# Performance work log

Measured on AMD Instinct MI355X. Metric: run time of the kernel, lower is better.

The kernel has to match this reference:

```python
import jax, jax.numpy as jnp
import numpy as np

B, T, D = 2, 2048, 2048
N_HEADS, N_KV = 16, 4
HD = D // N_HEADS  # 128
ROPE_BASE = 10000.0


def _rope_tables(t, dim, base=ROPE_BASE):
    inv_freq = 1.0 / (base ** (jnp.arange(0, dim, 2, dtype=jnp.float32) / dim))
    freqs = jnp.arange(t, dtype=jnp.float32)[:, None] * inv_freq[None, :]  # (T, dim/2)
    emb = jnp.concatenate([freqs, freqs], axis=-1)  # (T, dim)
    return jnp.cos(emb), jnp.sin(emb)


def _rotate_half(x):
    x1, x2 = jnp.split(x, 2, axis=-1)
    return jnp.concatenate([-x2, x1], axis=-1)


def _apply_rope(x, cos, sin):
    # x: (B, H, T, hd); cos/sin: (T, hd)
    return x * cos[None, None] + _rotate_half(x) * sin[None, None]


def setup_inputs() -> dict:
    key = jax.random.key(0)
    ks = jax.random.split(key, 5)
    s = 0.02
    return {
        "x": jax.random.normal(ks[0], (B, T, D), jnp.float32),
        "wq": jax.random.normal(ks[1], (D, N_HEADS * HD), jnp.float32) * s,
        "wk": jax.random.normal(ks[2], (D, N_KV * HD), jnp.float32) * s,
        "wv": jax.random.normal(ks[3], (D, N_KV * HD), jnp.float32) * s,
        "wo": jax.random.normal(ks[4], (D, D), jnp.float32) * s,
    }


def reference(x, wq, wk, wv, wo):
    b, t, c = x.shape
    n_rep = N_HEADS // N_KV
    scale = 1.0 / np.sqrt(HD)

    q = (x @ wq).reshape(b, t, N_HEADS, HD).transpose(0, 2, 1, 3)  # (B,H,T,hd)
    k = (x @ wk).reshape(b, t, N_KV, HD).transpose(0, 2, 1, 3)     # (B,Hkv,T,hd)
    v = (x @ wv).reshape(b, t, N_KV, HD).transpose(0, 2, 1, 3)

    cos, sin = _rope_tables(t, HD)
    q = _apply_rope(q, cos, sin)
    k = _apply_rope(k, cos, sin)

    # repeat_kv (GQA)
    k = jnp.repeat(k, n_rep, axis=1)  # (B,H,T,hd)
    v = jnp.repeat(v, n_rep, axis=1)

    scores = jnp.einsum("bhqd,bhkd->bhqk", q, k) * scale
    causal = jnp.tril(jnp.ones((t, t), dtype=bool))
    scores = jnp.where(causal[None, None], scores, -jnp.inf)
    attn = jax.nn.softmax(scores, axis=-1)
    out = jnp.einsum("bhqk,bhkd->bhqd", attn, v)
    out = out.transpose(0, 2, 1, 3).reshape(b, t, c)
    return out @ wo
```

## Files before the change

kernel.cpp:

```cpp
#include <hip/hip_runtime.h>
#include <hip/hip_bf16.h>
#include <math.h>

#define B_   2
#define T_   2048
#define D_   2048
#define NH_  16
#define NKV_ 4
#define HD_  128
#define MROWS (B_*T_)
#define NQKV  (NH_*HD_ + 2*NKV_*HD_)

typedef __bf16 bf16_t;
typedef __bf16 bf16x8 __attribute__((ext_vector_type(8)));
typedef __bf16 bf16x4 __attribute__((ext_vector_type(4)));
typedef float  floatx4 __attribute__((ext_vector_type(4)));

__device__ __forceinline__ void async_copy16(const bf16_t* gsrc, bf16_t* ldst) {
  __builtin_amdgcn_global_load_lds(
      (const __attribute__((address_space(1))) unsigned int*)gsrc,
      (__attribute__((address_space(3))) unsigned int*)ldst, 16, 0, 0);
}

__global__ void prep_fused(const float* __restrict__ s0, const float* __restrict__ s1,
                           const float* __restrict__ s2, const float* __restrict__ s3,
                           const float* __restrict__ sx,
                           bf16_t* __restrict__ d0, bf16_t* __restrict__ d1,
                           bf16_t* __restrict__ d2, bf16_t* __restrict__ d3,
                           bf16_t* __restrict__ dx) {
  const int z = blockIdx.z;
  const int tx = threadIdx.x, ty = threadIdx.y;
  if (z == 4) {
    int i = ((blockIdx.y * 64 + blockIdx.x) * 256 + ty * 32 + tx) * 8;
    float4 a = *(const float4*)(sx + i);
    float4 b = *(const float4*)(sx + i + 4);
    bf16x8 v;
    v[0]=(bf16_t)a.x; v[1]=(bf16_t)a.y; v[2]=(bf16_t)a.z; v[3]=(bf16_t)a.w;
    v[4]=(bf16_t)b.x; v[5]=(bf16_t)b.y; v[6]=(bf16_t)b.z; v[7]=(bf16_t)b.w;
    *(bf16x8*)(dx + i) = v;
    return;
  }
  const int N = (z == 1 || z == 2) ? 512 : 2048;
  const int n0 = blockIdx.x * 32;
  if (n0 >= N) return;
  const float* src = (z == 0) ? s0 : (z == 1) ? s1 : (z == 2) ? s2 : s3;
  bf16_t*      dst = (z == 0) ? d0 : (z == 1) ? d1 : (z == 2) ? d2 : d3;
  const int K = 2048;
  __shared__ float tile[32][33];
  int k0 = blockIdx.y * 32;
#pragma unroll
  for (int r = 0; r < 4; r++)
    tile[ty + r*8][tx] = src[(size_t)(k0 + ty + r*8) * N + n0 + tx];
  __syncthreads();
#pragma unroll
  for (int r = 0; r < 4; r++)
    dst[(size_t)(n0 + ty + r*8) * K + k0 + tx] = (bf16_t)tile[tx][ty + r*8];
}

template <typename OUT_T>
__global__ __launch_bounds__(256, 3)
void gemm_bt(const bf16_t* __restrict__ A, const bf16_t* __restrict__ Bt,
             OUT_T* __restrict__ C, int M, int N, int K) {
  __shared__ __align__(16) bf16_t As[128 * 64];
  __shared__ __align__(16) bf16_t Bs[128 * 64];
  const int tid  = threadIdx.x;
  const int wave = tid >> 6, lane = tid & 63;
  const int quad = lane >> 4, l16 = lane & 15;
  const int nBlocksM = M >> 7;
  const int bm = blockIdx.x % nBlocksM, bn = blockIdx.x / nBlocksM;
  const int m0 = bm * 128, n0 = bn * 128;
  const int wm = (wave >> 1) * 64, wn = (wave & 1) * 64;

  floatx4 acc[4][4];
#pragma unroll
  for (int i = 0; i < 4; i++)
#pragma unroll
    for (int j = 0; j < 4; j++) acc[i][j] = floatx4{0.f, 0.f, 0.f, 0.f};

  for (int k0 = 0; k0 < K; k0 += 64) {
    __syncthreads();
#pragma unroll
    for (int i = 0; i < 4; i++) {
      int e = i * 256 + tid;
      int row = e >> 3, grp = e & 7;
      int gg = grp ^ (row & 7);
      async_copy16(A + (size_t)(m0 + row) * K + k0 + gg * 8, As + e * 8);
    }
#pragma unroll
    for (int i = 0; i < 4; i++) {
      int e = i * 256 + tid;
      int row = e >> 3, grp = e & 7;
      int gg = grp ^ (row & 7);
      async_copy16(Bt + (size_t)(n0 + row) * K + k0 + gg * 8, Bs + e * 8);
    }
    __syncthreads();
#pragma unroll
    for (int ks = 0; ks < 2; ks++) {
      bf16x8 af[4], bfr[4];
      int grp = ks * 4 + quad;
#pragma unroll
      for (int mi = 0; mi < 4; mi++) {
        int row = wm + mi * 16 + l16;
        af[mi] = *(const bf16x8*)(As + row * 64 + ((grp ^ (row & 7)) << 3));
      }
#pragma unroll
      for (int ni = 0; ni < 4; ni++) {
        int row = wn + ni * 16 + l16;
        bfr[ni] = *(const bf16x8*)(Bs + row * 64 + ((grp ^ (row & 7)) << 3));
      }
#pragma unroll
      for (int mi = 0; mi < 4; mi++)
#pragma unroll
        for (int ni = 0; ni < 4; ni++)
          acc[mi][ni] = __builtin_amdgcn_mfma_f32_16x16x32_bf16(af[mi], bfr[ni], acc[mi][ni], 0, 0, 0);
    }
  }
#pragma unroll
  for (int mi = 0; mi < 4; mi++) {
#pragma unroll
    for (int r = 0; r < 4; r++) {
      int row = m0 + wm + mi * 16 + quad * 4 + r;
      size_t base = (size_t)row * N + n0 + wn;
#pragma unroll
      for (int ni = 0; ni < 4; ni++)
        C[base + ni * 16 + l16] = (OUT_T)acc[mi][ni][r];
    }
  }
}

__global__ void rope_k(const bf16_t* __restrict__ qkv, bf16_t* __restrict__ Kb) {
  int g = blockIdx.x * 256 + threadIdx.x;
  int j = g & 63;
  int rest = g >> 6;
  int kvh = rest & 3;
  int row = rest >> 2;
  int t = row & (T_ - 1);
  int b = row >> 11;
  const bf16_t* src = qkv + (size_t)row * NQKV + NH_ * HD_ + kvh * HD_;
  float ang = (float)t * __expf(-0.14391156816f * (float)j);
  float sn, cs;
  __sincosf(ang, &sn, &cs);
  float x0 = (float)src[j];
  float x1 = (float)src[j + 64];
  bf16_t* dst = Kb + ((size_t)(b * NKV_ + kvh) * T_ + t) * HD_;
  dst[j]      = (bf16_t)(x0 * cs - x1 * sn);
  dst[j + 64] = (bf16_t)(x1 * cs + x0 * sn);
}

__global__ void v_transpose(const bf16_t* __restrict__ qkv, bf16_t* __restrict__ Vt) {
  __shared__ float tile[32][33];
  int t0 = blockIdx.x * 32, d0 = blockIdx.y * 32;
  int bk = blockIdx.z;
  int b = bk / NKV_, kvh = bk % NKV_;
  int tx = threadIdx.x, ty = threadIdx.y;
#pragma unroll
  for (int r = 0; r < 4; r++) {
    int t = t0 + ty + r * 8;
    tile[ty + r*8][tx] =
        (float)qkv[(size_t)(b * T_ + t) * NQKV + (NH_ + NKV_) * HD_ + kvh * HD_ + d0 + tx];
  }
  __syncthreads();
#pragma unroll
  for (int r = 0; r < 4; r++) {
    int d = d0 + ty + r * 8;
    Vt[((size_t)(b * NKV_ + kvh) * HD_ + d) * T_ + t0 + tx] = (bf16_t)tile[tx][ty + r*8];
  }
}

__global__ __launch_bounds__(256, 2)
void flash_attn(const bf16_t* __restrict__ qkv, const bf16_t* __restrict__ Kb,
                const bf16_t* __restrict__ Vt, bf16_t* __restrict__ Ob) {
  __shared__ __align__(16) bf16_t Ks[2][64 * 128];
  __shared__ __align__(16) bf16_t Vs[2][128 * 64];
  __shared__ __align__(16) bf16_t Ps[4][16 * 72];

  const int tid = threadIdx.x;
  const int wave = tid >> 6, lane = tid & 63;
  const int quad = lane >> 4, l16 = lane & 15;
  const int nQT = T_ / 64;
  const int bid = blockIdx.x;
  const int bh = bid % (B_ * NH_);
  const int qt = (nQT - 1) - (bid / (B_ * NH_));
  const int h = bh % NH_;
  const int b = bh / NH_;
  const int kv = h >> 2;

  const bf16_t* kbase = Kb + ((size_t)(b * NKV_ + kv) * T_) * HD_;
  const bf16_t* vbase = Vt + ((size_t)(b * NKV_ + kv) * HD_) * T_;

  auto stage = [&](int kt, int bufi) {
#pragma unroll
    for (int i = 0; i < 4; i++) {
      int e = i * 256 + tid;
      int row = e >> 4, grp = e & 15;
      int gg = grp ^ (row & 15);
      async_copy16(kbase + (size_t)(kt * 64 + row) * HD_ + gg * 8, &Ks[bufi][e * 8]);
    }
#pragma unroll
    for (int i = 0; i < 4; i++) {
      int e = i * 256 + tid;
      int row = e >> 3, grp = e & 7;
      int gg = grp ^ (row & 7);
      async_copy16(vbase + (size_t)row * T_ + kt * 64 + gg * 8, &Vs[bufi][e * 8]);
    }
  };

  stage(0, 0);

  bf16x8 qf[4];
  {
    const int t_row = qt * 64 + wave * 16 + l16;
    const bf16_t* qptr = qkv + (size_t)(b * T_ + t_row) * NQKV + h * HD_;
    bf16x8 qraw[4];
#pragma unroll
    for (int ks = 0; ks < 4; ks++)
      qraw[ks] = *(const bf16x8*)(qptr + ks * 32 + quad * 8);
    const float scale = 0.12751651541057752f;
#pragma unroll
    for (int ks = 0; ks < 2; ks++)
#pragma unroll
      for (int j = 0; j < 8; j++) {
        int d = ks * 32 + quad * 8 + j;
        float ang = (float)t_row * __expf(-0.14391156816f * (float)d);
        float sn, cs;
        __sincosf(ang, &sn, &cs);
        float lo = (float)qraw[ks][j], hi = (float)qraw[ks + 2][j];
        qf[ks][j]     = (bf16_t)((lo * cs - hi * sn) * scale);
        qf[ks + 2][j] = (bf16_t)((hi * cs + lo * sn) * scale);
      }
  }

  floatx4 o[8];
#pragma unroll
  for (int i = 0; i < 8; i++) o[i] = floatx4{0.f, 0.f, 0.f, 0.f};
  float m_s = -1e30f, l_s = 0.f;

  for (int kt = 0; kt <= qt; kt++) {
    const int bufi = kt & 1;
    __syncthreads();
    if (kt < qt) stage(kt + 1, bufi ^ 1);

    floatx4 s[4];
#pragma unroll
    for (int nt = 0; nt < 4; nt++) s[nt] = floatx4{0.f, 0.f, 0.f, 0.f};
#pragma unroll
    for (int ks = 0; ks < 4; ks++) {
      int grp = ks * 4 + quad;
#pragma unroll
      for (int nt = 0; nt < 4; nt++) {
        int row = nt * 16 + l16;
        bf16x8 kf = *(const bf16x8*)(&Ks[bufi][row * 128 + ((grp ^ (row & 15)) << 3)]);
        s[nt] = __builtin_amdgcn_mfma_f32_16x16x32_bf16(kf, qf[ks], s[nt], 0, 0, 0);
      }
    }

    if (kt == qt) {
      int qlocal = wave * 16 + l16;
#pragma unroll
      for (int nt = 0; nt < 4; nt++)
#pragma unroll
        for (int r = 0; r < 4; r++) {
          int klocal = nt * 16 + quad * 4 + r;
          if (klocal > qlocal) s[nt][r] = -1e30f;
        }
    }

    float mx = fmaxf(fmaxf(s[0][0], s[0][1]), fmaxf(s[0][2], s[0][3]));
#pragma unroll
    for (int nt = 1; nt < 4; nt++)
      mx = fmaxf(mx, fmaxf(fmaxf(s[nt][0], s[nt][1]), fmaxf(s[nt][2], s[nt][3])));
    mx = fmaxf(mx, __shfl_xor(mx, 16, 64));
    mx = fmaxf(mx, __shfl_xor(mx, 32, 64));
    float mnew = fmaxf(m_s, mx);
    float alpha = __builtin_amdgcn_exp2f(m_s - mnew);
    m_s = mnew;
    float sum = 0.f;
#pragma unroll
    for (int nt = 0; nt < 4; nt++)
#pragma unroll
      for (int r = 0; r < 4; r++) {
        float p = __builtin_amdgcn_exp2f(s[nt][r] - mnew);
        s[nt][r] = p;
        sum += p;
      }
    sum += __shfl_xor(sum, 16, 64);
    sum += __shfl_xor(sum, 32, 64);
    l_s = l_s * alpha + sum;
#pragma unroll
    for (int dt = 0; dt < 8; dt++) o[dt] *= alpha;

#pragma unroll
    for (int nt = 0; nt < 4; nt++) {
      bf16x4 p4;
#pragma unroll
      for (int r = 0; r < 4; r++) p4[r] = (bf16_t)s[nt][r];
      *(bf16x4*)(&Ps[wave][l16 * 72 + nt * 16 + quad * 4]) = p4;
    }

#pragma unroll
    for (int ks = 0; ks < 2; ks++) {
      bf16x8 pf = *(const bf16x8*)(&Ps[wave][l16 * 72 + ks * 32 + quad * 8]);
      int grp = ks * 4 + quad;
#pragma unroll
      for (int dt = 0; dt < 8; dt++) {
        int row = dt * 16 + l16;
        bf16x8 vf = *(const bf16x8*)(&Vs[bufi][row * 64 + ((grp ^ (row & 7)) << 3)]);
        o[dt] = __builtin_amdgcn_mfma_f32_16x16x32_bf16(vf, pf, o[dt], 0, 0, 0);
      }
    }
  }

  {
    int qg = qt * 64 + wave * 16 + l16;
    float inv_l = 1.f / l_s;
    size_t base = ((size_t)(b * T_) + qg) * D_ + h * HD_;
#pragma unroll
    for (int dt = 0; dt < 8; dt++) {
      bf16x4 w;
#pragma unroll
      for (int r = 0; r < 4; r++) w[r] = (bf16_t)(o[dt][r] * inv_l);
      *(bf16x4*)(Ob + base + dt * 16 + quad * 4) = w;
    }
  }
}

extern "C" void kernel_launch(void* const* d_in, const int* in_sizes, int n_in,
                              void* d_out, int out_size, void* d_ws, size_t ws_size,
                              hipStream_t stream) {
  const float* x  = (const float*)d_in[0];
  const float* wq = (const float*)d_in[1];
  const float* wk = (const float*)d_in[2];
  const float* wv = (const float*)d_in[3];
  const float* wo = (const float*)d_in[4];
  float* out = (float*)d_out;

  bf16_t* x_bf   = (bf16_t*)d_ws;
  bf16_t* attn_o = x_bf;
  bf16_t* wqkv_t = x_bf + (size_t)MROWS * D_;
  bf16_t* wo_t   = wqkv_t + (size_t)NQKV * D_;
  bf16_t* qkv    = wo_t + (size_t)D_ * D_;
  bf16_t* Kb     = qkv + (size_t)MROWS * NQKV;
  bf16_t* Vt     = Kb + (size_t)B_ * NKV_ * T_ * HD_;

  prep_fused<<<dim3(64, 64, 5), dim3(32, 8), 0, stream>>>(
      wq, wk, wv, wo, x,
      wqkv_t, wqkv_t + (size_t)2048 * D_, wqkv_t + (size_t)2560 * D_, wo_t, x_bf);

  gemm_bt<bf16_t><<<(MROWS / 128) * (NQKV / 128), 256, 0, stream>>>(
      x_bf, wqkv_t, qkv, MROWS, NQKV, D_);

  rope_k<<<(MROWS * NKV_ * 64) / 256, 256, 0, stream>>>(qkv, Kb);
  v_transpose<<<dim3(T_ / 32, HD_ / 32, B_ * NKV_), dim3(32, 8), 0, stream>>>(qkv, Vt);

  flash_attn<<<B_ * NH_ * (T_ / 64), 256, 0, stream>>>(qkv, Kb, Vt, attn_o);

  gemm_bt<float><<<(MROWS / 128) * (D_ / 128), 256, 0, stream>>>(
      attn_o, wo_t, out, MROWS, D_, D_);
}
```

Before: 263.4 us.

## Fuse K-rope and V-transpose kernels, keep P in registers, lazy rescale in flash attention

Merges the rope_k and v_transpose launches into one kv_prep kernel that splits work by block index, removing one launch. In flash attention, the P tile no longer round-trips through LDS. Its register layout is reused directly as the MFMA operand, and the V reads are changed to two 4-element loads so they match the new k-ordering. Online-softmax rescaling of o and l is skipped unless the running max grows by more than a threshold, and s_setprio raises wave priority around the MFMA blocks. The threshold rescale relies on fp32 headroom for unnormalised exponentials, and the permuted V loads use narrower LDS reads.

```diff
diff --git a/kernel.cpp b/kernel.cpp
--- a/kernel.cpp
+++ b/kernel.cpp
@@ -128,31 +128,34 @@
   }
 }
 
-__global__ void rope_k(const bf16_t* __restrict__ qkv, bf16_t* __restrict__ Kb) {
-  int g = blockIdx.x * 256 + threadIdx.x;
-  int j = g & 63;
-  int rest = g >> 6;
-  int kvh = rest & 3;
-  int row = rest >> 2;
-  int t = row & (T_ - 1);
-  int b = row >> 11;
-  const bf16_t* src = qkv + (size_t)row * NQKV + NH_ * HD_ + kvh * HD_;
-  float ang = (float)t * __expf(-0.14391156816f * (float)j);
-  float sn, cs;
-  __sincosf(ang, &sn, &cs);
-  float x0 = (float)src[j];
-  float x1 = (float)src[j + 64];
-  bf16_t* dst = Kb + ((size_t)(b * NKV_ + kvh) * T_ + t) * HD_;
-  dst[j]      = (bf16_t)(x0 * cs - x1 * sn);
-  dst[j + 64] = (bf16_t)(x1 * cs + x0 * sn);
-}
-
-__global__ void v_transpose(const bf16_t* __restrict__ qkv, bf16_t* __restrict__ Vt) {
+#define ROPE_BLOCKS ((MROWS * NKV_ * 64) / 256)
+__global__ void kv_prep(const bf16_t* __restrict__ qkv, bf16_t* __restrict__ Kb,
+                        bf16_t* __restrict__ Vt) {
+  if (blockIdx.x < ROPE_BLOCKS) {
+    int g = blockIdx.x * 256 + threadIdx.x;
+    int j = g & 63;
+    int rest = g >> 6;
+    int kvh = rest & 3;
+    int row = rest >> 2;
+    int t = row & (T_ - 1);
+    int b = row >> 11;
+    const bf16_t* src = qkv + (size_t)row * NQKV + NH_ * HD_ + kvh * HD_;
+    float ang = (float)t * __expf(-0.14391156816f * (float)j);
+    float sn, cs;
+    __sincosf(ang, &sn, &cs);
+    float x0 = (float)src[j];
+    float x1 = (float)src[j + 64];
+    bf16_t* dst = Kb + ((size_t)(b * NKV_ + kvh) * T_ + t) * HD_;
+    dst[j]      = (bf16_t)(x0 * cs - x1 * sn);
+    dst[j + 64] = (bf16_t)(x1 * cs + x0 * sn);
+    return;
+  }
   __shared__ float tile[32][33];
-  int t0 = blockIdx.x * 32, d0 = blockIdx.y * 32;
-  int bk = blockIdx.z;
-  int b = bk / NKV_, kvh = bk % NKV_;
-  int tx = threadIdx.x, ty = threadIdx.y;
+  int bb = blockIdx.x - ROPE_BLOCKS;
+  int bx = bb & 63, by = (bb >> 6) & 3, bz = bb >> 8;
+  int t0 = bx * 32, d0 = by * 32;
+  int b = bz / NKV_, kvh = bz % NKV_;
+  int tx = threadIdx.x & 31, ty = threadIdx.x >> 5;
 #pragma unroll
   for (int r = 0; r < 4; r++) {
     int t = t0 + ty + r * 8;
@@ -172,7 +175,6 @@
                 const bf16_t* __restrict__ Vt, bf16_t* __restrict__ Ob) {
   __shared__ __align__(16) bf16_t Ks[2][64 * 128];
   __shared__ __align__(16) bf16_t Vs[2][128 * 64];
-  __shared__ __align__(16) bf16_t Ps[4][16 * 72];
 
   const int tid = threadIdx.x;
   const int wave = tid >> 6, lane = tid & 63;
@@ -243,6 +245,7 @@
     floatx4 s[4];
 #pragma unroll
     for (int nt = 0; nt < 4; nt++) s[nt] = floatx4{0.f, 0.f, 0.f, 0.f};
+    __builtin_amdgcn_s_setprio(1);
 #pragma unroll
     for (int ks = 0; ks < 4; ks++) {
       int grp = ks * 4 + quad;
@@ -253,6 +256,7 @@
         s[nt] = __builtin_amdgcn_mfma_f32_16x16x32_bf16(kf, qf[ks], s[nt], 0, 0, 0);
       }
     }
+    __builtin_amdgcn_s_setprio(0);
 
     if (kt == qt) {
       int qlocal = wave * 16 + l16;
@@ -271,43 +275,51 @@
       mx = fmaxf(mx, fmaxf(fmaxf(s[nt][0], s[nt][1]), fmaxf(s[nt][2], s[nt][3])));
     mx = fmaxf(mx, __shfl_xor(mx, 16, 64));
     mx = fmaxf(mx, __shfl_xor(mx, 32, 64));
-    float mnew = fmaxf(m_s, mx);
-    float alpha = __builtin_amdgcn_exp2f(m_s - mnew);
-    m_s = mnew;
+    if (!__all(mx <= m_s + 8.0f)) {
+      float mnew = fmaxf(m_s, mx);
+      float alpha = __builtin_amdgcn_exp2f(m_s - mnew);
+      m_s = mnew;
+      l_s *= alpha;
+#pragma unroll
+      for (int dt = 0; dt < 8; dt++) o[dt] *= alpha;
+    }
     float sum = 0.f;
 #pragma unroll
     for (int nt = 0; nt < 4; nt++)
 #pragma unroll
       for (int r = 0; r < 4; r++) {
-        float p = __builtin_amdgcn_exp2f(s[nt][r] - mnew);
+        float p = __builtin_amdgcn_exp2f(s[nt][r] - m_s);
         s[nt][r] = p;
         sum += p;
       }
     sum += __shfl_xor(sum, 16, 64);
     sum += __shfl_xor(sum, 32, 64);
-    l_s = l_s * alpha + sum;
-#pragma unroll
-    for (int dt = 0; dt < 8; dt++) o[dt] *= alpha;
-
-#pragma unroll
-    for (int nt = 0; nt < 4; nt++) {
-      bf16x4 p4;
-#pragma unroll
-      for (int r = 0; r < 4; r++) p4[r] = (bf16_t)s[nt][r];
-      *(bf16x4*)(&Ps[wave][l16 * 72 + nt * 16 + quad * 4]) = p4;
-    }
-
+    l_s += sum;
+
+    __builtin_amdgcn_s_setprio(1);
 #pragma unroll
     for (int ks = 0; ks < 2; ks++) {
-      bf16x8 pf = *(const bf16x8*)(&Ps[wave][l16 * 72 + ks * 32 + quad * 8]);
-      int grp = ks * 4 + quad;
+      bf16x8 pf;
+#pragma unroll
+      for (int j = 0; j < 4; j++) {
+        pf[j]     = (bf16_t)s[ks][j];
+        pf[j + 4] = (bf16_t)s[ks + 2][j];
+      }
+      const int glo = 2 * ks + (quad >> 1);
+      const int ghi = glo + 4;
+      const int half = (quad & 1) * 4;
 #pragma unroll
       for (int dt = 0; dt < 8; dt++) {
         int row = dt * 16 + l16;
-        bf16x8 vf = *(const bf16x8*)(&Vs[bufi][row * 64 + ((grp ^ (row & 7)) << 3)]);
+        int sw = row & 7;
+        const bf16_t* vrow = &Vs[bufi][row * 64];
+        bf16x4 vlo = *(const bf16x4*)(vrow + (((glo ^ sw) << 3) + half));
+        bf16x4 vhi = *(const bf16x4*)(vrow + (((ghi ^ sw) << 3) + half));
+        bf16x8 vf = __builtin_shufflevector(vlo, vhi, 0, 1, 2, 3, 4, 5, 6, 7);
         o[dt] = __builtin_amdgcn_mfma_f32_16x16x32_bf16(vf, pf, o[dt], 0, 0, 0);
       }
     }
+    __builtin_amdgcn_s_setprio(0);
   }
 
   {
@@ -349,8 +361,8 @@
   gemm_bt<bf16_t><<<(MROWS / 128) * (NQKV / 128), 256, 0, stream>>>(
       x_bf, wqkv_t, qkv, MROWS, NQKV, D_);
 
-  rope_k<<<(MROWS * NKV_ * 64) / 256, 256, 0, stream>>>(qkv, Kb);
-  v_transpose<<<dim3(T_ / 32, HD_ / 32, B_ * NKV_), dim3(32, 8), 0, stream>>>(qkv, Vt);
+  kv_prep<<<ROPE_BLOCKS + (T_ / 32) * (HD_ / 32) * B_ * NKV_, 256, 0, stream>>>(
+      qkv, Kb, Vt);
 
   flash_attn<<<B_ * NH_ * (T_ / 64), 256, 0, stream>>>(qkv, Kb, Vt, attn_o);
 
```

Result: slower. 286.0 us (+8.6%).
